# Kernel optimization log

Measured on AMD Instinct MI355X. Metric: run time of the kernel, lower is better.

Reference implementation:

```python
import jax, jax.numpy as jnp
import numpy as np

NUM_TOKENS = 32768   # flat token count across the batch
HIDDEN = 2048
IVS = 32000          # initial (base) vocab size
SLOTS = 64           # hyper weight pool slots
MAX_HYPER = 1024     # hyper tokens per pool slot
BATCH = 64           # number of requests


def setup_inputs() -> dict:
    key = jax.random.key(0)
    k1, k2, k3, k4, k5 = jax.random.split(key, 5)
    input_ = jax.random.randint(k1, (NUM_TOKENS,), 0, IVS + MAX_HYPER, dtype=jnp.int32)
    token_to_batch_indices = jax.random.randint(k2, (NUM_TOKENS,), 0, BATCH, dtype=jnp.int32)
    hyper_weight_pool_indices = jax.random.randint(k3, (BATCH,), 0, SLOTS, dtype=jnp.int32)
    weight = jax.random.normal(k4, (IVS, HIDDEN), dtype=jnp.float32) * 0.02
    embedding_buffer = jax.random.normal(k5, (SLOTS, MAX_HYPER, HIDDEN), dtype=jnp.float32) * 0.02
    return {
        "input_": input_,
        "token_to_batch_indices": token_to_batch_indices,
        "hyper_weight_pool_indices": hyper_weight_pool_indices,
        "weight": weight,
        "embedding_buffer": embedding_buffer,
    }


def reference(input_, token_to_batch_indices, hyper_weight_pool_indices, weight, embedding_buffer):
    ivs = weight.shape[0]
    base_mask = input_ < ivs                      # [N] bool
    base_ids = jnp.where(base_mask, input_, 0)    # input_ * base_mask.long()
    hyper_ids = jnp.where(base_mask, 0, input_ - ivs)

    # masked base embedding lookup
    base_emb = weight[base_ids] * base_mask[:, None].astype(weight.dtype)   # [N, H]

    # per-token pool slot: batch index -> pool slot
    pool_slots = hyper_weight_pool_indices[token_to_batch_indices]          # [N]

    # hyper embedding gather with in-range guard (token_id < buffer.shape[1])
    in_range = hyper_ids < embedding_buffer.shape[1]
    safe_ids = jnp.where(in_range, hyper_ids, 0)
    hyper_mask = ((~base_mask) & in_range)[:, None].astype(weight.dtype)
    hyper_emb = embedding_buffer[pool_slots, safe_ids] * hyper_mask         # [N, H]

    return base_emb + hyper_emb
```

## Files before the change

### kernel.cpp

```cpp
#include <hip/hip_runtime.h>

#define NUM_TOKENS 32768
#define HIDDEN     2048
#define IVS        32000
#define SLOTS      64
#define MAX_HYPER  1024

typedef float f32x4 __attribute__((ext_vector_type(4)));

__global__ __launch_bounds__(256)
void zip2zip_embed_kernel(const int*   __restrict__ input_,
                          const int*   __restrict__ t2b,
                          const int*   __restrict__ pool_idx,
                          const float* __restrict__ weight,
                          const float* __restrict__ ebuf,
                          float*       __restrict__ out)
{
    const int wave  = threadIdx.x >> 6;
    const int lane  = threadIdx.x & 63;
    const int token = (blockIdx.x << 2) + wave;

    const int id = input_[token];

    const f32x4* src = nullptr;
    if (id < IVS) {
        src = reinterpret_cast<const f32x4*>(weight + (size_t)id * HIDDEN);
    } else {
        const int hid = id - IVS;
        if (hid < MAX_HYPER) {
            const int slot = pool_idx[t2b[token]];
            src = reinterpret_cast<const f32x4*>(
                ebuf + ((size_t)slot * MAX_HYPER + (size_t)hid) * HIDDEN);
        }
    }

    f32x4* dst = reinterpret_cast<f32x4*>(out + (size_t)token * HIDDEN);
    constexpr int NV = HIDDEN / 4;

    if (src) {
        f32x4 v[8];
        #pragma unroll
        for (int j = 0; j < 8; ++j) {
            v[j] = src[lane + j * 64];
        }
        #pragma unroll
        for (int j = 0; j < 8; ++j) {
            __builtin_nontemporal_store(v[j], &dst[lane + j * 64]);
        }
    } else {
        const f32x4 z = {0.f, 0.f, 0.f, 0.f};
        #pragma unroll
        for (int j = 0; j < 8; ++j) {
            __builtin_nontemporal_store(z, &dst[lane + j * 64]);
        }
    }
    (void)NV;
}

extern "C" void kernel_launch(void* const* d_in, const int* in_sizes, int n_in,
                              void* d_out, int out_size, void* d_ws, size_t ws_size,
                              hipStream_t stream) {
    const int*   input_ = (const int*)d_in[0];
    const int*   t2b    = (const int*)d_in[1];
    const int*   pool   = (const int*)d_in[2];
    const float* weight = (const float*)d_in[3];
    const float* ebuf   = (const float*)d_in[4];
    float*       out    = (float*)d_out;

    zip2zip_embed_kernel<<<NUM_TOKENS / 4, 256, 0, stream>>>(
        input_, t2b, pool, weight, ebuf, out);
}
```

Before: 82.50 us.

## Counting-sort tokens by id so duplicate embedding rows are read adjacently

Adds a histogram, prefix-scan and scatter pass that sorts token indices by vocabulary id, then runs the copy kernel in sorted order so tokens sharing a row are fetched close together in time and hit in cache. The aim is to cut redundant DRAM reads of the weight table. In exchange it adds four extra launches, a single-block scan, and atomics. Output writes become scattered in row order, though each row is still written contiguously. Falls back to the direct kernel if the workspace is too small.

```diff
diff --git a/kernel.cpp b/kernel.cpp
--- a/kernel.cpp
+++ b/kernel.cpp
@@ -5,20 +5,90 @@
 #define IVS        32000
 #define SLOTS      64
 #define MAX_HYPER  1024
+#define BINS       (IVS + MAX_HYPER)
 
 typedef float f32x4 __attribute__((ext_vector_type(4)));
 
+
 __global__ __launch_bounds__(256)
-void zip2zip_embed_kernel(const int*   __restrict__ input_,
-                          const int*   __restrict__ t2b,
-                          const int*   __restrict__ pool_idx,
-                          const float* __restrict__ weight,
-                          const float* __restrict__ ebuf,
-                          float*       __restrict__ out)
+void zero_hist_kernel(int* __restrict__ hist) {
+    int i = blockIdx.x * 256 + threadIdx.x;
+    if (i < BINS) hist[i] = 0;
+}
+
+__global__ __launch_bounds__(256)
+void hist_kernel(const int* __restrict__ input_, int* __restrict__ hist) {
+    int t = blockIdx.x * 256 + threadIdx.x;
+    if (t < NUM_TOKENS) {
+        int id = input_[t];
+        if (id < 0) id = 0; else if (id >= BINS) id = BINS - 1;
+        atomicAdd(&hist[id], 1);
+    }
+}
+
+#define SCAN_T 1024
+#define SCAN_C ((BINS + SCAN_T - 1) / SCAN_T)
+
+__global__ __launch_bounds__(SCAN_T)
+void scan_kernel(int* __restrict__ hist) {
+    __shared__ int tot[SCAN_T];
+    const int t = threadIdx.x;
+    const int base = t * SCAN_C;
+
+    int sum = 0;
+    for (int i = 0; i < SCAN_C; ++i) {
+        int idx = base + i;
+        if (idx < BINS) sum += hist[idx];
+    }
+    tot[t] = sum;
+    __syncthreads();
+
+    for (int off = 1; off < SCAN_T; off <<= 1) {
+        int v = 0;
+        if (t >= off) v = tot[t - off];
+        __syncthreads();
+        if (t >= off) tot[t] += v;
+        __syncthreads();
+    }
+    int run = tot[t] - sum;
+
+    for (int i = 0; i < SCAN_C; ++i) {
+        int idx = base + i;
+        if (idx < BINS) {
+            int v = hist[idx];
+            hist[idx] = run;
+            run += v;
+        }
+    }
+}
+
+__global__ __launch_bounds__(256)
+void scatter_kernel(const int* __restrict__ input_,
+                    int* __restrict__ cursor,
+                    int* __restrict__ sorted) {
+    int t = blockIdx.x * 256 + threadIdx.x;
+    if (t < NUM_TOKENS) {
+        int id = input_[t];
+        if (id < 0) id = 0; else if (id >= BINS) id = BINS - 1;
+        int pos = atomicAdd(&cursor[id], 1);
+        sorted[pos] = t;
+    }
+}
+
+
+__global__ __launch_bounds__(256)
+void copy_kernel(const int*   __restrict__ sorted,
+                 const int*   __restrict__ input_,
+                 const int*   __restrict__ t2b,
+                 const int*   __restrict__ pool_idx,
+                 const float* __restrict__ weight,
+                 const float* __restrict__ ebuf,
+                 float*       __restrict__ out)
 {
     const int wave  = threadIdx.x >> 6;
     const int lane  = threadIdx.x & 63;
-    const int token = (blockIdx.x << 2) + wave;
+    const int gidx  = (blockIdx.x << 2) + wave;
+    const int token = sorted[gidx];
 
     const int id = input_[token];
 
@@ -35,26 +105,61 @@
     }
 
     f32x4* dst = reinterpret_cast<f32x4*>(out + (size_t)token * HIDDEN);
-    constexpr int NV = HIDDEN / 4;
 
     if (src) {
         f32x4 v[8];
         #pragma unroll
-        for (int j = 0; j < 8; ++j) {
-            v[j] = src[lane + j * 64];
-        }
+        for (int j = 0; j < 8; ++j) v[j] = src[lane + j * 64];
         #pragma unroll
-        for (int j = 0; j < 8; ++j) {
+        for (int j = 0; j < 8; ++j)
             __builtin_nontemporal_store(v[j], &dst[lane + j * 64]);
-        }
     } else {
         const f32x4 z = {0.f, 0.f, 0.f, 0.f};
         #pragma unroll
-        for (int j = 0; j < 8; ++j) {
+        for (int j = 0; j < 8; ++j)
             __builtin_nontemporal_store(z, &dst[lane + j * 64]);
+    }
+}
+
+
+__global__ __launch_bounds__(256)
+void copy_direct_kernel(const int*   __restrict__ input_,
+                        const int*   __restrict__ t2b,
+                        const int*   __restrict__ pool_idx,
+                        const float* __restrict__ weight,
+                        const float* __restrict__ ebuf,
+                        float*       __restrict__ out)
+{
+    const int wave  = threadIdx.x >> 6;
+    const int lane  = threadIdx.x & 63;
+    const int token = (blockIdx.x << 2) + wave;
+
+    const int id = input_[token];
+    const f32x4* src = nullptr;
+    if (id < IVS) {
+        src = reinterpret_cast<const f32x4*>(weight + (size_t)id * HIDDEN);
+    } else {
+        const int hid = id - IVS;
+        if (hid < MAX_HYPER) {
+            const int slot = pool_idx[t2b[token]];
+            src = reinterpret_cast<const f32x4*>(
+                ebuf + ((size_t)slot * MAX_HYPER + (size_t)hid) * HIDDEN);
         }
     }
-    (void)NV;
+    f32x4* dst = reinterpret_cast<f32x4*>(out + (size_t)token * HIDDEN);
+    if (src) {
+        f32x4 v[8];
+        #pragma unroll
+        for (int j = 0; j < 8; ++j) v[j] = src[lane + j * 64];
+        #pragma unroll
+        for (int j = 0; j < 8; ++j)
+            __builtin_nontemporal_store(v[j], &dst[lane + j * 64]);
+    } else {
+        const f32x4 z = {0.f, 0.f, 0.f, 0.f};
+        #pragma unroll
+        for (int j = 0; j < 8; ++j)
+            __builtin_nontemporal_store(z, &dst[lane + j * 64]);
+    }
 }
 
 extern "C" void kernel_launch(void* const* d_in, const int* in_sizes, int n_in,
@@ -67,6 +172,19 @@
     const float* ebuf   = (const float*)d_in[4];
     float*       out    = (float*)d_out;
 
-    zip2zip_embed_kernel<<<NUM_TOKENS / 4, 256, 0, stream>>>(
-        input_, t2b, pool, weight, ebuf, out);
+    const size_t need = (size_t)BINS * 4 + (size_t)NUM_TOKENS * 4;
+    if (ws_size >= need) {
+        int* hist   = (int*)d_ws;
+        int* sorted = hist + BINS;
+
+        zero_hist_kernel<<<(BINS + 255) / 256, 256, 0, stream>>>(hist);
+        hist_kernel<<<NUM_TOKENS / 256, 256, 0, stream>>>(input_, hist);
+        scan_kernel<<<1, SCAN_T, 0, stream>>>(hist);
+        scatter_kernel<<<NUM_TOKENS / 256, 256, 0, stream>>>(input_, hist, sorted);
+        copy_kernel<<<NUM_TOKENS / 4, 256, 0, stream>>>(
+            sorted, input_, t2b, pool, weight, ebuf, out);
+    } else {
+        copy_direct_kernel<<<NUM_TOKENS / 4, 256, 0, stream>>>(
+            input_, t2b, pool, weight, ebuf, out);
+    }
 }
```

Result: slower. 138.0 us (+67.3%).
